# Optimization experiments

Hardware: AMD Instinct MI355X
Metric: run time of the kernel (lower is better)

Reference implementation:

```python
import jax, jax.numpy as jnp
import numpy as np

NC = 10      # num_classes
HID = 64     # hidden_layer_dim
CIN = 512    # input_channels
THRESH = 100 # _LABEL2MASK_THRESHOL


def setup_inputs() -> dict:
    key = jax.random.key(0)
    k = jax.random.split(key, 5)
    B, h, w = 4, 60, 80
    feature1 = jax.random.normal(k[0], (B, CIN, h, w), jnp.float32)
    feature2 = jax.random.normal(k[1], (B, CIN, h // 2, w // 2), jnp.float32)
    s_in = (2.0 / CIN) ** 0.5   # kaiming_normal_ fan_in for 1x1 conv
    s_h = (2.0 / HID) ** 0.5
    w1 = jax.random.normal(k[2], (HID, CIN), jnp.float32) * s_in
    b1 = jnp.zeros((HID,), jnp.float32)
    w2 = jax.random.normal(k[3], (HID, CIN), jnp.float32) * s_in
    b2 = jnp.zeros((HID,), jnp.float32)
    w3 = jax.random.normal(k[4], (NC + 1, HID), jnp.float32) * s_h
    b3 = jnp.zeros((NC + 1,), jnp.float32)
    return {"feature1": feature1, "feature2": feature2,
            "w1": w1, "b1": b1, "w2": w2, "b2": b2, "w3": w3, "b3": b3}


def _resize_bilinear(x, H, W):
    # torch nn.Upsample(mode='bilinear', align_corners=False) ~ jax.image.resize bilinear
    B, C = x.shape[0], x.shape[1]
    return jax.image.resize(x, (B, C, H, W), method="bilinear")


def _label2bbx(seg):
    # Vectorized replacement of the batch x class Python loop: fused masked
    # min/max reductions per (batch, class). Classes 1..NC-1, class 0 skipped,
    # exactly as in the original. Fixed output shape (B*(NC-1), 6); rows with
    # pixel count < THRESH are filled with -1 (jit-compatible padding).
    B, H, W = seg.shape
    cls = jnp.arange(1, NC)                                   # (NC-1,)
    mask = seg[:, None, :, :] == cls[None, :, None, None]     # (B, NC-1, H, W)
    xs = jnp.arange(W)
    ys = jnp.arange(H)
    count = mask.sum(axis=(-2, -1))                           # (B, NC-1)
    xmin = jnp.min(jnp.where(mask, xs[None, None, None, :], W), axis=(-2, -1))
    xmax = jnp.max(jnp.where(mask, xs[None, None, None, :], -1), axis=(-2, -1))
    ymin = jnp.min(jnp.where(mask, ys[None, None, :, None], H), axis=(-2, -1))
    ymax = jnp.max(jnp.where(mask, ys[None, None, :, None], -1), axis=(-2, -1))
    bids = jnp.broadcast_to(jnp.arange(B)[:, None], (B, NC - 1))
    clsb = jnp.broadcast_to(cls[None, :], (B, NC - 1))
    bbx = jnp.stack([bids, xmin, ymin, xmax, ymax, clsb], axis=-1)  # (B, NC-1, 6)
    valid = (count >= THRESH)[..., None]
    return jnp.where(valid, bbx, -1).reshape(B * (NC - 1), 6)


def reference(feature1, feature2, w1, b1, w2, b2, w3, b3):
    # 1x1 convs expressed as channel GEMMs
    f1 = jax.nn.relu(jnp.einsum('bchw,oc->bohw', feature1, w1) + b1[None, :, None, None])
    f2 = jax.nn.relu(jnp.einsum('bchw,oc->bohw', feature2, w2) + b2[None, :, None, None])
    h, w = feature1.shape[2], feature1.shape[3]
    f2 = _resize_bilinear(f2, h, w)           # Upsample x2
    inter = f1 + f2
    up = _resize_bilinear(inter, 8 * h, 8 * w)  # Upsample x8
    logits = jax.nn.relu(jnp.einsum('bchw,oc->bohw', up, w3) + b3[None, :, None, None])
    probability = jax.nn.softmax(logits, axis=1)   # Softmax2d = softmax over C
    segmentation = jnp.argmax(probability, axis=1)  # (B, H, W)
    bbx = _label2bbx(segmentation)
    return probability, segmentation, bbx
```

## Files before the change

### kernel.cpp

```cpp
#include <hip/hip_runtime.h>

#define DEVINL __device__ __forceinline__

namespace {

constexpr int NB   = 4;
constexpr int CINv = 512;
constexpr int HIDv = 64;
constexpr int NCl  = 11;
constexpr int h1v = 60, w1v = 80;
constexpr int h2v = 30, w2v = 40;
constexpr int Hf = 480, Wf = 640;
constexpr int PPB1 = h1v * w1v;
constexpr int PPB2 = h2v * w2v;
constexpr int NP1 = NB * PPB1;
constexpr int NP2 = NB * PPB2;
constexpr int PPBF = Hf * Wf;
constexpr int NPF = NB * PPBF;

constexpr size_t WS_P1  = 0;
constexpr size_t WS_P2  = WS_P1 + 2ull * HIDv * NP1;
constexpr size_t WS_Z   = WS_P2 + 2ull * HIDv * NP2;
constexpr size_t WS_BBX = WS_Z + (size_t)NB * NCl * PPB1;

constexpr size_t OUT_SEG = (size_t)NB * NCl * PPBF;
constexpr size_t OUT_BBX = OUT_SEG + (size_t)NPF;

DEVINL int iclamp(int v, int lo, int hi) { return v < lo ? lo : (v > hi ? hi : v); }

template <int PPB>
DEVINL void gemm_tile(const float* __restrict__ F, const float* __restrict__ Wt,
                      float* __restrict__ P, int npix, int tile, int khalf,
                      float* A_lds , float* W_lds ) {
  const int t = threadIdx.x;
  const int pg = t & 15;
  const int og = t >> 4;
  const int gp0 = tile * 64;
  const int c0 = khalf * 256;

  float acc[4][4];
#pragma unroll
  for (int i = 0; i < 4; ++i)
#pragma unroll
    for (int j = 0; j < 4; ++j) acc[i][j] = 0.f;

  for (int kb = 0; kb < 8; ++kb) {
    const int cb = c0 + kb * 32;
    __syncthreads();
#pragma unroll
    for (int e = 0; e < 8; ++e) {
      int idx = e * 256 + t;
      int cc = idx >> 6, px = idx & 63;
      int gp = gp0 + px;
      int b = gp / PPB, pb = gp % PPB;
      A_lds[idx] = F[((size_t)b * CINv + (cb + cc)) * PPB + pb];
    }
#pragma unroll
    for (int e = 0; e < 8; ++e) {
      int idx = e * 256 + t;
      int o = idx >> 5, cc = idx & 31;
      W_lds[cc * 68 + o] = Wt[o * CINv + cb + cc];
    }
    __syncthreads();
#pragma unroll
    for (int cc = 0; cc < 32; ++cc) {
      float4 a = *reinterpret_cast<const float4*>(&A_lds[cc * 64 + pg * 4]);
      float4 w = *reinterpret_cast<const float4*>(&W_lds[cc * 68 + og * 4]);
      float av[4] = {a.x, a.y, a.z, a.w};
      float wv[4] = {w.x, w.y, w.z, w.w};
#pragma unroll
      for (int i = 0; i < 4; ++i)
#pragma unroll
        for (int j = 0; j < 4; ++j)
          acc[i][j] = fmaf(av[i], wv[j], acc[i][j]);
    }
  }
#pragma unroll
  for (int j = 0; j < 4; ++j) {
    int o = og * 4 + j;
    float4 v;
    v.x = acc[0][j]; v.y = acc[1][j]; v.z = acc[2][j]; v.w = acc[3][j];
    *reinterpret_cast<float4*>(&P[((size_t)khalf * HIDv + o) * npix + gp0 + pg * 4]) = v;
  }
}

__global__ __launch_bounds__(256) void k_gemm(const float* __restrict__ f1,
                                              const float* __restrict__ f2,
                                              const float* __restrict__ w1,
                                              const float* __restrict__ w2,
                                              float* __restrict__ ws) {
  __shared__ float A_lds[32 * 64];
  __shared__ float W_lds[32 * 68];
  const int bid = blockIdx.x;

  if (bid == 0 && threadIdx.x < 180) {
    int entry = threadIdx.x / 5, f = threadIdx.x % 5;
    int v = (f == 0) ? 0 : ((f == 1 || f == 3) ? 0x7fffffff : (int)0x80000000);
    reinterpret_cast<int*>(ws + WS_BBX)[entry * 32 + f] = v;
  }

  if (bid < 600) {
    gemm_tile<PPB1>(f1, w1, ws + WS_P1, NP1, bid >> 1, bid & 1, A_lds, W_lds);
  } else {
    int tt = bid - 600;
    gemm_tile<PPB2>(f2, w2, ws + WS_P2, NP2, tt >> 1, tt & 1, A_lds, W_lds);
  }
}

__global__ __launch_bounds__(256) void k_combine_z(const float* __restrict__ ws_ro,
                                                   float* __restrict__ ws,
                                                   const float* __restrict__ b1,
                                                   const float* __restrict__ b2,
                                                   const float* __restrict__ w3,
                                                   const float* __restrict__ b3) {
  __shared__ float inter[64 * 64];
  const int t = threadIdx.x;
  const int pxl = t & 63;
  const int qi = t >> 6;
  const int gp = blockIdx.x * 64 + pxl;
  const int b = gp / PPB1, pb = gp % PPB1;
  const int y = pb / w1v, x = pb % w1v;

  const float sx = x * 0.5f - 0.25f;
  const float x0f = floorf(sx);
  const float fx = sx - x0f;
  const int ix0 = iclamp((int)x0f, 0, w2v - 1);
  const int ix1 = iclamp((int)x0f + 1, 0, w2v - 1);
  const float sy = y * 0.5f - 0.25f;
  const float y0f = floorf(sy);
  const float fy = sy - y0f;
  const int iy0 = iclamp((int)y0f, 0, h2v - 1);
  const int iy1 = iclamp((int)y0f + 1, 0, h2v - 1);

  const float* p1 = ws_ro + WS_P1;
  const float* p2 = ws_ro + WS_P2;
  const int base2 = b * PPB2;
  const int i00 = base2 + iy0 * w2v + ix0;
  const int i01 = base2 + iy0 * w2v + ix1;
  const int i10 = base2 + iy1 * w2v + ix0;
  const int i11 = base2 + iy1 * w2v + ix1;

#pragma unroll
  for (int cc = 0; cc < 16; ++cc) {
    const int ch = qi * 16 + cc;
    float v = p1[(size_t)ch * NP1 + gp] + p1[(size_t)(HIDv + ch) * NP1 + gp] + b1[ch];
    v = fmaxf(v, 0.f);
    const float* pa = p2 + (size_t)ch * NP2;
    const float* pbp = p2 + (size_t)(HIDv + ch) * NP2;
    const float bb = b2[ch];
    float v00 = fmaxf(pa[i00] + pbp[i00] + bb, 0.f);
    float v01 = fmaxf(pa[i01] + pbp[i01] + bb, 0.f);
    float v10 = fmaxf(pa[i10] + pbp[i10] + bb, 0.f);
    float v11 = fmaxf(pa[i11] + pbp[i11] + bb, 0.f);
    float top = v00 + fx * (v01 - v00);
    float bot = v10 + fx * (v11 - v10);
    v += top + fy * (bot - top);
    inter[ch * 64 + pxl] = v;
  }
  __syncthreads();

  const int o0 = qi * 3;
  const int ocnt = (qi == 3) ? 2 : 3;
  float* z = ws + WS_Z;
  for (int oo = 0; oo < ocnt; ++oo) {
    const int o = o0 + oo;
    float acc = b3[o];
#pragma unroll
    for (int ch = 0; ch < 64; ++ch)
      acc = fmaf(inter[ch * 64 + pxl], w3[o * HIDv + ch], acc);
    z[((size_t)b * NCl + o) * PPB1 + pb] = acc;
  }
}

__global__ __launch_bounds__(256) void k_up_softmax(const float* __restrict__ ws,
                                                    float* __restrict__ out) {
  constexpr int ZR = 3, ZC = 18, ZN = NCl * ZR * ZC;
  __shared__ float zt[ZN];
  const int t = threadIdx.x;
  const int tile = blockIdx.x;
  const int tx = tile % 5;
  const int ty = (tile / 5) % 240;
  const int b  = tile / 1200;
  const int base_x = tx * 16 - 1;
  const int row0 = ty * 2;
  const int base_y = (int)floorf((row0 + 0.5f) * 0.125f - 0.5f);

  const float* zb = ws + WS_Z + (size_t)b * NCl * PPB1;
  for (int e = t; e < ZN; e += 256) {
    int ch = e / (ZR * ZC);
    int rc = e % (ZR * ZC);
    int row = rc / ZC, col = rc % ZC;
    int gr = iclamp(base_y + row, 0, h1v - 1);
    int gc = iclamp(base_x + col, 0, w1v - 1);
    zt[e] = zb[(size_t)ch * PPB1 + gr * w1v + gc];
  }
  __syncthreads();

  const int x  = t & 127;
  const int rr = t >> 7;
  const int X = tx * 128 + x;
  const int Y = row0 + rr;

  const float sy = (Y + 0.5f) * 0.125f - 0.5f;
  const int y0g = (int)floorf(sy);
  const float fy = sy - (float)y0g;
  const int lry = y0g - base_y;
  const int lcx = (2 * x + 9) >> 4;
  const float fx = (float)(2 * x - 7) * 0.0625f + 1.0f - (float)lcx;

  float lg[NCl];
  float m = -1.f;
  int bi = 0;
#pragma unroll
  for (int c = 0; c < NCl; ++c) {
    const int base = c * (ZR * ZC) + lry * ZC + lcx;
    float v00 = zt[base],      v01 = zt[base + 1];
    float v10 = zt[base + ZC], v11 = zt[base + ZC + 1];
    float l0 = v00 + fy * (v10 - v00);
    float l1 = v01 + fy * (v11 - v01);
    float v = fmaxf(l0 + fx * (l1 - l0), 0.f);
    lg[c] = v;
    if (v > m) { m = v; bi = c; }
  }

  float s = 0.f;
#pragma unroll
  for (int c = 0; c < NCl; ++c) {
    float e = __expf(lg[c] - m);
    lg[c] = e;
    s += e;
  }
  const float inv = __builtin_amdgcn_rcpf(s);

  const size_t r = (size_t)Y * Wf + X;
  float* prob = out + (size_t)b * NCl * PPBF;
#pragma unroll
  for (int c = 0; c < NCl; ++c)
    prob[(size_t)c * PPBF + r] = lg[c] * inv;
  out[OUT_SEG + (size_t)b * PPBF + r] = (float)bi;
}

__global__ __launch_bounds__(256) void k_bbx(const float* __restrict__ seg,
                                             int* __restrict__ acc) {
  __shared__ int sC[10], sXn[10], sXx[10], sYn[10], sYx[10];
  const int t = threadIdx.x;
  const int lane = t & 63, w = t >> 6;
  const int b = blockIdx.x / 120;
  const int rg = blockIdx.x % 120;
  const int row = rg * 4 + w;
  if (t < 10) {
    sC[t] = 0;
    sXn[t] = 0x7fffffff; sXx[t] = (int)0x80000000;
    sYn[t] = 0x7fffffff; sYx[t] = (int)0x80000000;
  }
  __syncthreads();

  int cnt[10], xmn[10], xmx[10];
#pragma unroll
  for (int c = 1; c <= 9; ++c) { cnt[c] = 0; xmn[c] = 0x7fffffff; xmx[c] = -1; }

  const float* srow = seg + (size_t)b * PPBF + (size_t)row * Wf;
  for (int ch = 0; ch < 10; ++ch) {
    const int cls = (int)srow[ch * 64 + lane];
#pragma unroll
    for (int c = 1; c <= 9; ++c) {
      unsigned long long msk = __ballot(cls == c);
      if (msk) {
        cnt[c] += (int)__popcll(msk);
        xmn[c] = min(xmn[c], ch * 64 + (int)__builtin_ctzll(msk));
        xmx[c] = max(xmx[c], ch * 64 + 63 - (int)__builtin_clzll(msk));
      }
    }
  }

  if (lane == 0) {
#pragma unroll
    for (int c = 1; c <= 9; ++c) {
      if (cnt[c]) {
        atomicAdd(&sC[c], cnt[c]);
        atomicMin(&sXn[c], xmn[c]);
        atomicMax(&sXx[c], xmx[c]);
        atomicMin(&sYn[c], row);
        atomicMax(&sYx[c], row);
      }
    }
  }
  __syncthreads();
  if (t >= 1 && t <= 9 && sC[t] > 0) {
    int* e = acc + (b * 9 + (t - 1)) * 32;
    atomicAdd(e + 0, sC[t]);
    atomicMin(e + 1, sXn[t]);
    atomicMax(e + 2, sXx[t]);
    atomicMin(e + 3, sYn[t]);
    atomicMax(e + 4, sYx[t]);
  }
}

__global__ void k_bbx_final(const int* __restrict__ acc, float* __restrict__ out) {
  const int t = threadIdx.x;
  if (t >= 36) return;
  const int* e = acc + t * 32;
  float* o = out + OUT_BBX + t * 6;
  if (e[0] >= 100) {
    o[0] = (float)(t / 9);
    o[1] = (float)e[1];
    o[2] = (float)e[3];
    o[3] = (float)e[2];
    o[4] = (float)e[4];
    o[5] = (float)(t % 9 + 1);
  } else {
    for (int i = 0; i < 6; ++i) o[i] = -1.f;
  }
}

}

extern "C" void kernel_launch(void* const* d_in, const int* in_sizes, int n_in,
                              void* d_out, int out_size, void* d_ws, size_t ws_size,
                              hipStream_t stream) {
  const float* f1 = (const float*)d_in[0];
  const float* f2 = (const float*)d_in[1];
  const float* w1 = (const float*)d_in[2];
  const float* b1 = (const float*)d_in[3];
  const float* w2 = (const float*)d_in[4];
  const float* b2 = (const float*)d_in[5];
  const float* w3 = (const float*)d_in[6];
  const float* b3 = (const float*)d_in[7];
  float* out = (float*)d_out;
  float* ws = (float*)d_ws;

  hipLaunchKernelGGL(k_gemm, dim3(750), dim3(256), 0, stream, f1, f2, w1, w2, ws);
  hipLaunchKernelGGL(k_combine_z, dim3(300), dim3(256), 0, stream, ws, ws, b1, b2, w3, b3);
  hipLaunchKernelGGL(k_up_softmax, dim3(4800), dim3(256), 0, stream, ws, out);
  hipLaunchKernelGGL(k_bbx, dim3(480), dim3(256), 0, stream, out + OUT_SEG,
                     (int*)(ws + WS_BBX));
  hipLaunchKernelGGL(k_bbx_final, dim3(1), dim3(64), 0, stream,
                     (const int*)(ws + WS_BBX), out);
}
```

Measured before the change: 69.48 us.

## Fuse bbox reduction into softmax, double-buffer GEMM with async LDS loads

The bounding-box reduction now happens inside the upsample/softmax kernel. Each wave ballots its argmax classes, and the block writes per-class partials to sharded atomic slots. This removes a separate pass that re-read the segmentation output. The GEMM now double-buffers its tiles, loading activations asynchronously from global memory into LDS and prefetching weights through registers, so loads overlap compute. The combine kernel uses 32-pixel blocks with w3 cached in LDS, and the bbox-init moves there. The changes add LDS use and atomic work per softmax block, and the final kernel now merges sixteen shards.

```diff
diff --git a/kernel.cpp b/kernel.cpp
--- a/kernel.cpp
+++ b/kernel.cpp
@@ -17,6 +17,7 @@
 constexpr int NP2 = NB * PPB2;
 constexpr int PPBF = Hf * Wf;
 constexpr int NPF = NB * PPBF;
+constexpr int NSHARD = 16;
 
 constexpr size_t WS_P1  = 0;
 constexpr size_t WS_P2  = WS_P1 + 2ull * HIDv * NP1;
@@ -28,53 +29,91 @@
 
 DEVINL int iclamp(int v, int lo, int hi) { return v < lo ? lo : (v > hi ? hi : v); }
 
+DEVINL void async_copy16(float* lds_dst, const float* g_src) {
+  __builtin_amdgcn_global_load_lds(
+      (const __attribute__((address_space(1))) unsigned int*)g_src,
+      (__attribute__((address_space(3))) unsigned int*)lds_dst, 16, 0, 0);
+}
+
 template <int PPB>
 DEVINL void gemm_tile(const float* __restrict__ F, const float* __restrict__ Wt,
                       float* __restrict__ P, int npix, int tile, int khalf,
-                      float* A_lds , float* W_lds ) {
+                      float* Ash , float* Wsh ) {
   const int t = threadIdx.x;
+  const int lane = t & 63;
+  const int wv = t >> 6;
   const int pg = t & 15;
   const int og = t >> 4;
   const int gp0 = tile * 64;
   const int c0 = khalf * 256;
 
+  const float* asrc[2];
+  float* adst[2][2];
+#pragma unroll
+  for (int i = 0; i < 2; ++i) {
+    const int E = wv * 512 + i * 256 + lane * 4;
+    const int cc = E >> 6, px = E & 63;
+    const int gp = gp0 + px;
+    const int bb = gp / PPB, pb = gp - bb * PPB;
+    asrc[i] = F + ((size_t)bb * CINv + cc) * PPB + pb;
+    adst[0][i] = Ash + 0 * 2048 + wv * 512 + i * 256;
+    adst[1][i] = Ash + 1 * 2048 + wv * 512 + i * 256;
+  }
+  const int wo = t >> 5, wc = t & 31;
+  const float* wsrc = Wt + (size_t)wo * CINv + wc;
+
   float acc[4][4];
 #pragma unroll
   for (int i = 0; i < 4; ++i)
 #pragma unroll
     for (int j = 0; j < 4; ++j) acc[i][j] = 0.f;
 
+  {
+    float wr[8];
+#pragma unroll
+    for (int e = 0; e < 8; ++e) wr[e] = wsrc[(size_t)e * 8 * CINv + c0];
+#pragma unroll
+    for (int i = 0; i < 2; ++i)
+      async_copy16(adst[0][i], asrc[i] + (size_t)c0 * PPB);
+#pragma unroll
+    for (int e = 0; e < 8; ++e) Wsh[wc * 68 + e * 8 + wo] = wr[e];
+  }
+  __syncthreads();
+
+#pragma unroll 2
   for (int kb = 0; kb < 8; ++kb) {
-    const int cb = c0 + kb * 32;
+    const int cur = kb & 1;
+    float wr[8];
+    if (kb < 7) {
+      const int cb = c0 + (kb + 1) * 32;
+#pragma unroll
+      for (int e = 0; e < 8; ++e) wr[e] = wsrc[(size_t)e * 8 * CINv + cb];
+#pragma unroll
+      for (int i = 0; i < 2; ++i)
+        async_copy16(adst[cur ^ 1][i], asrc[i] + (size_t)cb * PPB);
+    }
+    const float* Ab = Ash + cur * 2048;
+    const float* Wb = Wsh + cur * (32 * 68);
+#pragma unroll
+    for (int cc = 0; cc < 32; ++cc) {
+      float4 a = *reinterpret_cast<const float4*>(&Ab[cc * 64 + pg * 4]);
+      float4 w = *reinterpret_cast<const float4*>(&Wb[cc * 68 + og * 4]);
+      float av[4] = {a.x, a.y, a.z, a.w};
+      float wvv[4] = {w.x, w.y, w.z, w.w};
+#pragma unroll
+      for (int i = 0; i < 4; ++i)
+#pragma unroll
+        for (int j = 0; j < 4; ++j)
+          acc[i][j] = fmaf(av[i], wvv[j], acc[i][j]);
+    }
+    if (kb < 7) {
+      float* Wn = Wsh + (cur ^ 1) * (32 * 68);
+#pragma unroll
+      for (int e = 0; e < 8; ++e) Wn[wc * 68 + e * 8 + wo] = wr[e];
+    }
     __syncthreads();
-#pragma unroll
-    for (int e = 0; e < 8; ++e) {
-      int idx = e * 256 + t;
-      int cc = idx >> 6, px = idx & 63;
-      int gp = gp0 + px;
-      int b = gp / PPB, pb = gp % PPB;
-      A_lds[idx] = F[((size_t)b * CINv + (cb + cc)) * PPB + pb];
-    }
-#pragma unroll
-    for (int e = 0; e < 8; ++e) {
-      int idx = e * 256 + t;
-      int o = idx >> 5, cc = idx & 31;
-      W_lds[cc * 68 + o] = Wt[o * CINv + cb + cc];
-    }
-    __syncthreads();
-#pragma unroll
-    for (int cc = 0; cc < 32; ++cc) {
-      float4 a = *reinterpret_cast<const float4*>(&A_lds[cc * 64 + pg * 4]);
-      float4 w = *reinterpret_cast<const float4*>(&W_lds[cc * 68 + og * 4]);
-      float av[4] = {a.x, a.y, a.z, a.w};
-      float wv[4] = {w.x, w.y, w.z, w.w};
-#pragma unroll
-      for (int i = 0; i < 4; ++i)
-#pragma unroll
-        for (int j = 0; j < 4; ++j)
-          acc[i][j] = fmaf(av[i], wv[j], acc[i][j]);
-    }
-  }
+  }
+
 #pragma unroll
   for (int j = 0; j < 4; ++j) {
     int o = og * 4 + j;
@@ -89,37 +128,41 @@
                                               const float* __restrict__ w1,
                                               const float* __restrict__ w2,
                                               float* __restrict__ ws) {
-  __shared__ float A_lds[32 * 64];
-  __shared__ float W_lds[32 * 68];
+  __shared__ float Ash[2 * 2048];
+  __shared__ float Wsh[2 * 32 * 68];
   const int bid = blockIdx.x;
-
-  if (bid == 0 && threadIdx.x < 180) {
-    int entry = threadIdx.x / 5, f = threadIdx.x % 5;
-    int v = (f == 0) ? 0 : ((f == 1 || f == 3) ? 0x7fffffff : (int)0x80000000);
-    reinterpret_cast<int*>(ws + WS_BBX)[entry * 32 + f] = v;
-  }
-
   if (bid < 600) {
-    gemm_tile<PPB1>(f1, w1, ws + WS_P1, NP1, bid >> 1, bid & 1, A_lds, W_lds);
+    gemm_tile<PPB1>(f1, w1, ws + WS_P1, NP1, bid >> 1, bid & 1, Ash, Wsh);
   } else {
     int tt = bid - 600;
-    gemm_tile<PPB2>(f2, w2, ws + WS_P2, NP2, tt >> 1, tt & 1, A_lds, W_lds);
-  }
-}
-
-__global__ __launch_bounds__(256) void k_combine_z(const float* __restrict__ ws_ro,
-                                                   float* __restrict__ ws,
+    gemm_tile<PPB2>(f2, w2, ws + WS_P2, NP2, tt >> 1, tt & 1, Ash, Wsh);
+  }
+}
+
+__global__ __launch_bounds__(256) void k_combine_z(float* __restrict__ ws,
                                                    const float* __restrict__ b1,
                                                    const float* __restrict__ b2,
                                                    const float* __restrict__ w3,
                                                    const float* __restrict__ b3) {
-  __shared__ float inter[64 * 64];
+  __shared__ float inter[64 * 32];
+  __shared__ float w3s[NCl * HIDv];
   const int t = threadIdx.x;
-  const int pxl = t & 63;
-  const int qi = t >> 6;
-  const int gp = blockIdx.x * 64 + pxl;
-  const int b = gp / PPB1, pb = gp % PPB1;
-  const int y = pb / w1v, x = pb % w1v;
+
+  if (blockIdx.x == 0) {
+    int* sh = (int*)(ws + WS_BBX);
+    for (int i = t; i < NSHARD * 36 * 8; i += 256) {
+      int f = i & 7;
+      sh[i] = (f == 0 || f >= 5) ? 0
+            : ((f == 1 || f == 3) ? 0x7fffffff : (int)0x80000000);
+    }
+  }
+  for (int e = t; e < NCl * HIDv; e += 256) w3s[e] = w3[e];
+
+  const int pxl = t & 31;
+  const int qi = t >> 5;
+  const int gp = blockIdx.x * 32 + pxl;
+  const int b = gp / PPB1, pb = gp - b * PPB1;
+  const int y = pb / w1v, x = pb - y * w1v;
 
   const float sx = x * 0.5f - 0.25f;
   const float x0f = floorf(sx);
@@ -132,8 +175,8 @@
   const int iy0 = iclamp((int)y0f, 0, h2v - 1);
   const int iy1 = iclamp((int)y0f + 1, 0, h2v - 1);
 
-  const float* p1 = ws_ro + WS_P1;
-  const float* p2 = ws_ro + WS_P2;
+  const float* p1 = ws + WS_P1;
+  const float* p2 = ws + WS_P2;
   const int base2 = b * PPB2;
   const int i00 = base2 + iy0 * w2v + ix0;
   const int i01 = base2 + iy0 * w2v + ix1;
@@ -141,8 +184,8 @@
   const int i11 = base2 + iy1 * w2v + ix1;
 
 #pragma unroll
-  for (int cc = 0; cc < 16; ++cc) {
-    const int ch = qi * 16 + cc;
+  for (int cc = 0; cc < 8; ++cc) {
+    const int ch = qi * 8 + cc;
     float v = p1[(size_t)ch * NP1 + gp] + p1[(size_t)(HIDv + ch) * NP1 + gp] + b1[ch];
     v = fmaxf(v, 0.f);
     const float* pa = p2 + (size_t)ch * NP2;
@@ -155,27 +198,34 @@
     float top = v00 + fx * (v01 - v00);
     float bot = v10 + fx * (v11 - v10);
     v += top + fy * (bot - top);
-    inter[ch * 64 + pxl] = v;
+    inter[ch * 32 + pxl] = v;
   }
   __syncthreads();
 
-  const int o0 = qi * 3;
-  const int ocnt = (qi == 3) ? 2 : 3;
   float* z = ws + WS_Z;
-  for (int oo = 0; oo < ocnt; ++oo) {
-    const int o = o0 + oo;
-    float acc = b3[o];
+  {
+    float a = b3[qi];
 #pragma unroll
     for (int ch = 0; ch < 64; ++ch)
-      acc = fmaf(inter[ch * 64 + pxl], w3[o * HIDv + ch], acc);
-    z[((size_t)b * NCl + o) * PPB1 + pb] = acc;
+      a = fmaf(inter[ch * 32 + pxl], w3s[qi * HIDv + ch], a);
+    z[((size_t)b * NCl + qi) * PPB1 + pb] = a;
+  }
+  if (qi < 3) {
+    const int o = qi + 8;
+    float a = b3[o];
+#pragma unroll
+    for (int ch = 0; ch < 64; ++ch)
+      a = fmaf(inter[ch * 32 + pxl], w3s[o * HIDv + ch], a);
+    z[((size_t)b * NCl + o) * PPB1 + pb] = a;
   }
 }
 
 __global__ __launch_bounds__(256) void k_up_softmax(const float* __restrict__ ws,
-                                                    float* __restrict__ out) {
+                                                    float* __restrict__ out,
+                                                    int* __restrict__ shards) {
   constexpr int ZR = 3, ZC = 18, ZN = NCl * ZR * ZC;
   __shared__ float zt[ZN];
+  __shared__ int sB[4][9][4];
   const int t = threadIdx.x;
   const int tile = blockIdx.x;
   const int tx = tile % 5;
@@ -238,75 +288,69 @@
   for (int c = 0; c < NCl; ++c)
     prob[(size_t)c * PPBF + r] = lg[c] * inv;
   out[OUT_SEG + (size_t)b * PPBF + r] = (float)bi;
-}
-
-__global__ __launch_bounds__(256) void k_bbx(const float* __restrict__ seg,
-                                             int* __restrict__ acc) {
-  __shared__ int sC[10], sXn[10], sXx[10], sYn[10], sYx[10];
-  const int t = threadIdx.x;
-  const int lane = t & 63, w = t >> 6;
-  const int b = blockIdx.x / 120;
-  const int rg = blockIdx.x % 120;
-  const int row = rg * 4 + w;
-  if (t < 10) {
-    sC[t] = 0;
-    sXn[t] = 0x7fffffff; sXx[t] = (int)0x80000000;
-    sYn[t] = 0x7fffffff; sYx[t] = (int)0x80000000;
+
+  const int lane = t & 63;
+  const int wv = t >> 6;
+  int cw[9], xn[9], xx[9];
+#pragma unroll
+  for (int c = 1; c <= 9; ++c) {
+    unsigned long long msk = __ballot(bi == c);
+    cw[c - 1] = (int)__popcll(msk);
+    xn[c - 1] = msk ? (int)__builtin_ctzll(msk) : 0;
+    xx[c - 1] = msk ? 63 - (int)__builtin_clzll(msk) : 0;
+  }
+  if (lane == 0) {
+#pragma unroll
+    for (int c = 0; c < 9; ++c) {
+      sB[wv][c][0] = cw[c];
+      sB[wv][c][1] = X + xn[c];
+      sB[wv][c][2] = X + xx[c];
+      sB[wv][c][3] = Y;
+    }
   }
   __syncthreads();
-
-  int cnt[10], xmn[10], xmx[10];
-#pragma unroll
-  for (int c = 1; c <= 9; ++c) { cnt[c] = 0; xmn[c] = 0x7fffffff; xmx[c] = -1; }
-
-  const float* srow = seg + (size_t)b * PPBF + (size_t)row * Wf;
-  for (int ch = 0; ch < 10; ++ch) {
-    const int cls = (int)srow[ch * 64 + lane];
-#pragma unroll
-    for (int c = 1; c <= 9; ++c) {
-      unsigned long long msk = __ballot(cls == c);
-      if (msk) {
-        cnt[c] += (int)__popcll(msk);
-        xmn[c] = min(xmn[c], ch * 64 + (int)__builtin_ctzll(msk));
-        xmx[c] = max(xmx[c], ch * 64 + 63 - (int)__builtin_clzll(msk));
+  if (t < 9) {
+    int C = 0, mn = 0x7fffffff, mx = -1, yn = 0x7fffffff, yx = -1;
+#pragma unroll
+    for (int w2 = 0; w2 < 4; ++w2) {
+      int cc = sB[w2][t][0];
+      if (cc) {
+        C += cc;
+        mn = min(mn, sB[w2][t][1]); mx = max(mx, sB[w2][t][2]);
+        yn = min(yn, sB[w2][t][3]); yx = max(yx, sB[w2][t][3]);
       }
     }
-  }
-
-  if (lane == 0) {
-#pragma unroll
-    for (int c = 1; c <= 9; ++c) {
-      if (cnt[c]) {
-        atomicAdd(&sC[c], cnt[c]);
-        atomicMin(&sXn[c], xmn[c]);
-        atomicMax(&sXx[c], xmx[c]);
-        atomicMin(&sYn[c], row);
-        atomicMax(&sYx[c], row);
-      }
-    }
-  }
-  __syncthreads();
-  if (t >= 1 && t <= 9 && sC[t] > 0) {
-    int* e = acc + (b * 9 + (t - 1)) * 32;
-    atomicAdd(e + 0, sC[t]);
-    atomicMin(e + 1, sXn[t]);
-    atomicMax(e + 2, sXx[t]);
-    atomicMin(e + 3, sYn[t]);
-    atomicMax(e + 4, sYx[t]);
-  }
-}
-
-__global__ void k_bbx_final(const int* __restrict__ acc, float* __restrict__ out) {
+    if (C) {
+      int* e = shards + (((tile & (NSHARD - 1)) * 36) + b * 9 + t) * 8;
+      atomicAdd(e + 0, C);
+      atomicMin(e + 1, mn);
+      atomicMax(e + 2, mx);
+      atomicMin(e + 3, yn);
+      atomicMax(e + 4, yx);
+    }
+  }
+}
+
+__global__ void k_bbx_final(const int* __restrict__ sh, float* __restrict__ out) {
   const int t = threadIdx.x;
   if (t >= 36) return;
-  const int* e = acc + t * 32;
+  int C = 0, xn = 0x7fffffff, xx = -1, yn = 0x7fffffff, yx = -1;
+  for (int s = 0; s < NSHARD; ++s) {
+    const int* e = sh + (s * 36 + t) * 8;
+    int c = e[0];
+    if (c) {
+      C += c;
+      xn = min(xn, e[1]); xx = max(xx, e[2]);
+      yn = min(yn, e[3]); yx = max(yx, e[4]);
+    }
+  }
   float* o = out + OUT_BBX + t * 6;
-  if (e[0] >= 100) {
+  if (C >= 100) {
     o[0] = (float)(t / 9);
-    o[1] = (float)e[1];
-    o[2] = (float)e[3];
-    o[3] = (float)e[2];
-    o[4] = (float)e[4];
+    o[1] = (float)xn;
+    o[2] = (float)yn;
+    o[3] = (float)xx;
+    o[4] = (float)yx;
     o[5] = (float)(t % 9 + 1);
   } else {
     for (int i = 0; i < 6; ++i) o[i] = -1.f;
@@ -330,9 +374,8 @@
   float* ws = (float*)d_ws;
 
   hipLaunchKernelGGL(k_gemm, dim3(750), dim3(256), 0, stream, f1, f2, w1, w2, ws);
-  hipLaunchKernelGGL(k_combine_z, dim3(300), dim3(256), 0, stream, ws, ws, b1, b2, w3, b3);
-  hipLaunchKernelGGL(k_up_softmax, dim3(4800), dim3(256), 0, stream, ws, out);
-  hipLaunchKernelGGL(k_bbx, dim3(480), dim3(256), 0, stream, out + OUT_SEG,
+  hipLaunchKernelGGL(k_combine_z, dim3(600), dim3(256), 0, stream, ws, b1, b2, w3, b3);
+  hipLaunchKernelGGL(k_up_softmax, dim3(4800), dim3(256), 0, stream, ws, out,
                      (int*)(ws + WS_BBX));
   hipLaunchKernelGGL(k_bbx_final, dim3(1), dim3(64), 0, stream,
                      (const int*)(ws + WS_BBX), out);
```

Result: slower. 111.4 us (+60.3%).
